# Performance work log

Measured on AMD Instinct MI355X. Metric: run time of the kernel, lower is better.

The kernel has to match this reference:

```python
import jax, jax.numpy as jnp
import numpy as np

ALPHA = 0.2  # tf.nn.leaky_relu default alpha
B, LATENT, T, N = 8, 256, 128, 768
F, L, E = 4, 3, 12288


def _causal_conv1d(x, w, b):
    # x: [B,T,Cin], w: [K,Cin,Cout] -> causal pad left by K-1
    k = w.shape[0]
    y = jax.lax.conv_general_dilated(x, w, (1,), ((k - 1, 0),),
                                     dimension_numbers=('NWC', 'WIO', 'NWC'))
    return y + b


def _same_conv1d(x, w, b):
    y = jax.lax.conv_general_dilated(x, w, (1,), 'SAME',
                                     dimension_numbers=('NWC', 'WIO', 'NWC'))
    return y + b


def _same_conv2d(x, w, b):
    y = jax.lax.conv_general_dilated(x, w, (1, 1), 'SAME',
                                     dimension_numbers=('NHWC', 'HWIO', 'NHWC'))
    return y + b


def _gat(nodes, row, col, qw, qb, kw, kb, vw, vb):
    # tf_geometric-style single-head GAT; row/col already contain self-loops.
    M = nodes.shape[0]
    Q = jax.nn.leaky_relu(nodes @ qw + qb, ALPHA)
    K = jax.nn.leaky_relu(nodes @ kw + kb, ALPHA)
    V = nodes @ vw
    scale = jnp.sqrt(jnp.asarray(Q.shape[-1], nodes.dtype))
    score = jnp.sum(Q[row] * K[col], axis=-1) / scale  # [E']
    smax = jax.ops.segment_max(score, row, num_segments=M)
    ex = jnp.exp(score - smax[row])
    den = jax.ops.segment_sum(ex, row, num_segments=M)
    att = ex / den[row]
    out = jax.ops.segment_sum(V[col] * att[:, None], row, num_segments=M)
    return out + vb


def _gw_layer(y, row, col, wa, ba, wb, bb, qw, qb, kw, kb, vw, vb, rw, rb):
    b_, t_, n_, f_ = y.shape
    x = jnp.moveaxis(y, -1, 0)  # [F,B,T,N]

    def branch(xf, wa_, ba_, wb_, bb_, qw_, qb_, kw_, kb_, vw_, vb_):
        a = jax.nn.sigmoid(_causal_conv1d(xf, wa_, ba_))
        g = a * jnp.tanh(_causal_conv1d(xf, wb_, bb_))   # gated TCN [B,T,N]
        nodes = g.transpose(0, 2, 1).reshape(b_ * n_, t_)  # node id = b*N + n
        h = _gat(nodes, row, col, qw_, qb_, kw_, kb_, vw_, vb_)
        return h.reshape(b_, n_, t_).transpose(0, 2, 1)  # [B,T,N]

    outs = jax.vmap(branch)(x, wa, ba, wb, bb, qw, qb, kw, kb, vw, vb)
    outs = jnp.moveaxis(outs, 0, -1)                      # [B,T,N,F]
    res = jnp.einsum('btnf,fg->btng', y, rw) + rb         # 1x1 res conv
    return outs + res


def _decoder(x, edges, shunt_dense_w, shunt_dense_b, shunt_c1_w, shunt_c1_b,
             shunt_c2_w, shunt_c2_b, tcn_a_w, tcn_a_b, tcn_b_w, tcn_b_b,
             gat_q_w, gat_q_b, gat_k_w, gat_k_b, gat_v_w, gat_v_b,
             res_w, res_b, skip_w, skip_b, out1_w, out1_b, out2_w, out2_b):
    # ConvShunt: [B,latent] -> [B,T] -> [B,T,N] -> [B,T,N,F]
    y = x @ shunt_dense_w + shunt_dense_b
    y = _same_conv1d(y[..., None], shunt_c1_w, shunt_c1_b)
    y = _same_conv2d(y[..., None], shunt_c2_w, shunt_c2_b)
    M = B * N
    self_idx = jnp.arange(M, dtype=edges.dtype)
    row = jnp.concatenate([edges[0], self_idx])
    col = jnp.concatenate([edges[1], self_idx])
    skips = []
    for i in range(L):
        y = _gw_layer(y, row, col, tcn_a_w[i], tcn_a_b[i], tcn_b_w[i], tcn_b_b[i],
                      gat_q_w[i], gat_q_b[i], gat_k_w[i], gat_k_b[i],
                      gat_v_w[i], gat_v_b[i], res_w[i], res_b[i])
        skips.append(jax.nn.leaky_relu(
            jnp.einsum('btnf,f->btn', y, skip_w[i]) + skip_b[i], ALPHA))
    s = jnp.stack(skips, axis=-1)                         # [B,T,N,L]
    g = jax.nn.leaky_relu(_same_conv2d(s, out1_w, out1_b), ALPHA)
    return _same_conv2d(g, out2_w, out2_b)                # [B,T,N,1]


def setup_inputs() -> dict:
    ks = iter(jax.random.split(jax.random.key(0), 32))

    def w(shape, fan_in):
        return jax.random.normal(next(ks), shape, jnp.float32) / np.sqrt(fan_in).astype(np.float32)

    return {
        'x': jax.random.normal(next(ks), (B, LATENT), jnp.float32),
        'edges': jax.random.randint(next(ks), (2, E), 0, N, jnp.int32),
        'shunt_dense_w': w((LATENT, T), LATENT),
        'shunt_dense_b': jnp.zeros((T,), jnp.float32),
        'shunt_c1_w': w((3, 1, N), 3),
        'shunt_c1_b': jnp.zeros((N,), jnp.float32),
        'shunt_c2_w': w((3, 3, 1, F), 9),
        'shunt_c2_b': jnp.zeros((F,), jnp.float32),
        'tcn_a_w': w((L, F, 5, N, N), 5 * N),
        'tcn_a_b': jnp.zeros((L, F, N), jnp.float32),
        'tcn_b_w': w((L, F, 5, N, N), 5 * N),
        'tcn_b_b': jnp.zeros((L, F, N), jnp.float32),
        'gat_q_w': w((L, F, T, T), T),
        'gat_q_b': jnp.zeros((L, F, T), jnp.float32),
        'gat_k_w': w((L, F, T, T), T),
        'gat_k_b': jnp.zeros((L, F, T), jnp.float32),
        'gat_v_w': w((L, F, T, T), T),
        'gat_v_b': jnp.zeros((L, F, T), jnp.float32),
        'res_w': w((L, F, F), F),
        'res_b': jnp.zeros((L, F), jnp.float32),
        'skip_w': w((L, F), F),
        'skip_b': jnp.zeros((L,), jnp.float32),
        'out1_w': w((3, 3, L, 1), 9 * L),
        'out1_b': jnp.zeros((1,), jnp.float32),
        'out2_w': w((1, 1, 1, 1), 1),
        'out2_b': jnp.zeros((1,), jnp.float32),
    }


def reference(x, edges, shunt_dense_w, shunt_dense_b, shunt_c1_w, shunt_c1_b,
              shunt_c2_w, shunt_c2_b, tcn_a_w, tcn_a_b, tcn_b_w, tcn_b_b,
              gat_q_w, gat_q_b, gat_k_w, gat_k_b, gat_v_w, gat_v_b,
              res_w, res_b, skip_w, skip_b, out1_w, out1_b, out2_w, out2_b):
    return _decoder(x, edges, shunt_dense_w, shunt_dense_b, shunt_c1_w, shunt_c1_b,
                    shunt_c2_w, shunt_c2_b, tcn_a_w, tcn_a_b, tcn_b_w, tcn_b_b,
                    gat_q_w, gat_q_b, gat_k_w, gat_k_b, gat_v_w, gat_v_b,
                    res_w, res_b, skip_w, skip_b, out1_w, out1_b, out2_w, out2_b)
```

## Files before the change

### kernel.cpp

```cpp
#include <hip/hip_runtime.h>
#include <math.h>

#define ALPHA_ 0.2f
#define AS1 __attribute__((address_space(1)))
#define AS3 __attribute__((address_space(3)))

constexpr int B_ = 8, LATENT_ = 256, T_ = 128, N_ = 768, F_ = 4, L_ = 3, E_ = 12288;
constexpr int M_ = B_ * N_;
constexpr int MT_ = B_ * T_;
constexpr int EP_ = E_ + M_;
constexpr int BTN_ = B_ * T_ * N_;
constexpr size_t SZ_ = (size_t)BTN_ * F_;
constexpr int KTCN_ = 5 * N_;
constexpr int KSPLIT_ = KTCN_ / 2;
constexpr int TP_ = T_ + 4;

typedef __bf16 bf16x8 __attribute__((ext_vector_type(8)));
typedef float f32x4 __attribute__((ext_vector_type(4)));

__device__ __forceinline__ float lrelu(float x) { return x > 0.0f ? x : ALPHA_ * x; }
__device__ __forceinline__ unsigned short f2bf(float x) {
    union { __bf16 h; unsigned short u; } c; c.h = (__bf16)x; return c.u;
}

__global__ void k_dense(const float* __restrict__ x, const float* __restrict__ w,
                        const float* __restrict__ b, float* __restrict__ y0) {
    int i = blockIdx.x * blockDim.x + threadIdx.x;
    if (i >= B_ * T_) return;
    int bb = i / T_, t = i % T_;
    float acc = b[t];
    for (int l = 0; l < LATENT_; ++l) acc += x[bb * LATENT_ + l] * w[l * T_ + t];
    y0[i] = acc;
}

__global__ void k_conv1(const float* __restrict__ y0, const float* __restrict__ w,
                        const float* __restrict__ b, float* __restrict__ y1) {
    int i = blockIdx.x * blockDim.x + threadIdx.x;
    if (i >= BTN_) return;
    int n = i % N_, t = (i / N_) % T_, bb = i / (N_ * T_);
    float acc = b[n];
    #pragma unroll
    for (int k = 0; k < 3; ++k) {
        int tt = t - 1 + k;
        if (tt >= 0 && tt < T_) acc += y0[bb * T_ + tt] * w[k * N_ + n];
    }
    y1[i] = acc;
}

__global__ void k_conv2w(const float* __restrict__ y1, const float* __restrict__ w,
                         const float* __restrict__ b, float* __restrict__ y,
                         unsigned short* __restrict__ xTpad) {
    int i = blockIdx.x * blockDim.x + threadIdx.x;
    if (i >= BTN_) return;
    int n = i % N_, t = (i / N_) % T_, bb = i / (N_ * T_);
    float acc[F_];
    #pragma unroll
    for (int f = 0; f < F_; ++f) acc[f] = b[f];
    #pragma unroll
    for (int dt = 0; dt < 3; ++dt) {
        int tt = t - 1 + dt;
        if (tt < 0 || tt >= T_) continue;
        #pragma unroll
        for (int dn = 0; dn < 3; ++dn) {
            int nn = n - 1 + dn;
            if (nn < 0 || nn >= N_) continue;
            float v = y1[(bb * T_ + tt) * N_ + nn];
            #pragma unroll
            for (int f = 0; f < F_; ++f) acc[f] += v * w[(dt * 3 + dn) * F_ + f];
        }
    }
    #pragma unroll
    for (int f = 0; f < F_; ++f) {
        y[(size_t)i * F_ + f] = acc[f];
        xTpad[((size_t)(f * B_ + bb) * TP_ + 4 + t) * N_ + n] = f2bf(acc[f]);
    }
}

__global__ __launch_bounds__(256) void k_convT(const float* __restrict__ in,
        unsigned short* __restrict__ outT, int Kd, int Nd) {
    __shared__ float tl[32][33];
    const int f = blockIdx.z;
    in += (size_t)f * Kd * Nd;
    outT += (size_t)f * Kd * Nd;
    const int x0 = blockIdx.x * 32;
    const int y0 = blockIdx.y * 32;
    const int tx = threadIdx.x & 31, ty = threadIdx.x >> 5;
    #pragma unroll
    for (int r = 0; r < 4; ++r)
        tl[ty + r * 8][tx] = in[(size_t)(y0 + ty + r * 8) * Nd + x0 + tx];
    __syncthreads();
    #pragma unroll
    for (int r = 0; r < 4; ++r)
        outT[(size_t)(x0 + ty + r * 8) * Kd + y0 + tx] = f2bf(tl[tx][ty + r * 8]);
}

__global__ __launch_bounds__(256) void k_tcn_mfma(
        const unsigned short* __restrict__ xTpad,
        const unsigned short* __restrict__ wat, const unsigned short* __restrict__ wbt,
        const float* __restrict__ ba, const float* __restrict__ bbias,
        float* __restrict__ oa0, float* __restrict__ oa1,
        float* __restrict__ ob0, float* __restrict__ ob1) {
    __shared__ unsigned short As[128 * 32];
    __shared__ unsigned short Bs[128 * 32];
    const int zz = blockIdx.z;
    const int f = zz & 3;
    const int wsel = (zz >> 2) & 1;
    const int s = zz >> 3;
    const int n0 = blockIdx.x * 128;
    const int bt = blockIdx.y;
    const unsigned short* xf = xTpad + (size_t)(f * B_ + bt) * TP_ * N_;
    const unsigned short* wf = (wsel ? wbt : wat) + (size_t)f * N_ * KTCN_ + (size_t)n0 * KTCN_;
    const float* bias = (wsel ? bbias : ba) + f * N_;
    float* out = (wsel ? (s ? ob1 : ob0) : (s ? oa1 : oa0));
    const int tid = threadIdx.x;
    const int lane = tid & 63;
    const int w = tid >> 6;
    const int wm = (w >> 1) * 64, wn = (w & 1) * 64;
    const int r16 = lane & 15, kb = lane >> 4;
    const int srow = lane >> 2;
    const int scol = (lane & 3) * 8;
    f32x4 acc[4][4] = {};
    const int k_lo = s * KSPLIT_, k_hi = k_lo + KSPLIT_;
    for (int kk0 = k_lo; kk0 < k_hi; kk0 += 32) {
        const int ks = kk0 / N_;
        const int nin0 = kk0 - ks * N_;
        #pragma unroll
        for (int h = 0; h < 2; ++h) {
            const int seg = w + 4 * h;
            const int row = seg * 16 + srow;
            const unsigned short* gA = xf + (size_t)(row + ks) * N_ + nin0 + scol;
            const unsigned short* gB = wf + (size_t)row * KTCN_ + kk0 + scol;
            __builtin_amdgcn_global_load_lds((const AS1 unsigned int*)(const void*)gA,
                    (AS3 unsigned int*)(void*)(As + seg * 512), 16, 0, 0);
            __builtin_amdgcn_global_load_lds((const AS1 unsigned int*)(const void*)gB,
                    (AS3 unsigned int*)(void*)(Bs + seg * 512), 16, 0, 0);
        }
        __syncthreads();
        bf16x8 av[4], bv[4];
        #pragma unroll
        for (int i = 0; i < 4; ++i) av[i] = *(const bf16x8*)(As + (wm + i * 16 + r16) * 32 + kb * 8);
        #pragma unroll
        for (int j = 0; j < 4; ++j) bv[j] = *(const bf16x8*)(Bs + (wn + j * 16 + r16) * 32 + kb * 8);
        #pragma unroll
        for (int i = 0; i < 4; ++i)
            #pragma unroll
            for (int j = 0; j < 4; ++j)
                acc[i][j] = __builtin_amdgcn_mfma_f32_16x16x32_bf16(av[i], bv[j], acc[i][j], 0, 0, 0);
        __syncthreads();
    }
    float* of = out + (size_t)(f * B_ + bt) * T_ * N_;
    #pragma unroll
    for (int i = 0; i < 4; ++i) {
        #pragma unroll
        for (int j = 0; j < 4; ++j) {
            const int n = n0 + wn + j * 16 + r16;
            const float bv2 = (s == 0) ? bias[n] : 0.0f;
            #pragma unroll
            for (int r = 0; r < 4; ++r) {
                const int m = wm + i * 16 + kb * 4 + r;
                of[(size_t)m * N_ + n] = acc[i][j][r] + bv2;
            }
        }
    }
}

__global__ __launch_bounds__(256) void k_gate_nodes(const float* __restrict__ a0,
        const float* __restrict__ a1, const float* __restrict__ b0,
        const float* __restrict__ b1, unsigned short* __restrict__ nodes) {
    __shared__ float tl[32][33];
    const int bz = blockIdx.z;
    const int t0 = blockIdx.x * 32, n0 = blockIdx.y * 32;
    const int tx = threadIdx.x & 31, ty = threadIdx.x >> 5;
    const size_t base = (size_t)bz * T_ * N_;
    #pragma unroll
    for (int r = 0; r < 4; ++r) {
        const size_t idx = base + (size_t)(t0 + ty + r * 8) * N_ + n0 + tx;
        const float av = a0[idx] + a1[idx], bvv = b0[idx] + b1[idx];
        tl[ty + r * 8][tx] = (1.0f / (1.0f + __expf(-av))) * tanhf(bvv);
    }
    __syncthreads();
    #pragma unroll
    for (int r = 0; r < 4; ++r)
        nodes[base + (size_t)(n0 + ty + r * 8) * T_ + t0 + tx] = f2bf(tl[tx][ty + r * 8]);
}

__global__ __launch_bounds__(256) void k_proj_mfma(
        const unsigned short* __restrict__ nodes, const unsigned short* __restrict__ pwt,
        const float* __restrict__ qb, const float* __restrict__ kbias,
        float* __restrict__ Q, float* __restrict__ K, float* __restrict__ V) {
    __shared__ unsigned short As[128 * 32];
    __shared__ unsigned short Bs[128 * 32];
    const int zz = blockIdx.z;
    const int f = zz & 3;
    const int sel = zz >> 2;
    const int m0 = blockIdx.y * 128;
    const unsigned short* af = nodes + (size_t)f * M_ * T_;
    const unsigned short* wfp = pwt + (size_t)sel * F_ * T_ * T_ + (size_t)f * T_ * T_;
    const float* bias = (sel == 0) ? qb : (sel == 1 ? kbias : nullptr);
    float* out = (sel == 0) ? Q : (sel == 1 ? K : V);
    const int tid = threadIdx.x;
    const int lane = tid & 63;
    const int w = tid >> 6;
    const int wm = (w >> 1) * 64, wn = (w & 1) * 64;
    const int r16 = lane & 15, kb = lane >> 4;
    const int srow = lane >> 2;
    const int scol = (lane & 3) * 8;
    f32x4 acc[4][4] = {};
    for (int kk0 = 0; kk0 < T_; kk0 += 32) {
        #pragma unroll
        for (int h = 0; h < 2; ++h) {
            const int seg = w + 4 * h;
            const int row = seg * 16 + srow;
            const unsigned short* gA = af + (size_t)(m0 + row) * T_ + kk0 + scol;
            const unsigned short* gB = wfp + (size_t)row * T_ + kk0 + scol;
            __builtin_amdgcn_global_load_lds((const AS1 unsigned int*)(const void*)gA,
                    (AS3 unsigned int*)(void*)(As + seg * 512), 16, 0, 0);
            __builtin_amdgcn_global_load_lds((const AS1 unsigned int*)(const void*)gB,
                    (AS3 unsigned int*)(void*)(Bs + seg * 512), 16, 0, 0);
        }
        __syncthreads();
        bf16x8 av[4], bv[4];
        #pragma unroll
        for (int i = 0; i < 4; ++i) av[i] = *(const bf16x8*)(As + (wm + i * 16 + r16) * 32 + kb * 8);
        #pragma unroll
        for (int j = 0; j < 4; ++j) bv[j] = *(const bf16x8*)(Bs + (wn + j * 16 + r16) * 32 + kb * 8);
        #pragma unroll
        for (int i = 0; i < 4; ++i)
            #pragma unroll
            for (int j = 0; j < 4; ++j)
                acc[i][j] = __builtin_amdgcn_mfma_f32_16x16x32_bf16(av[i], bv[j], acc[i][j], 0, 0, 0);
        __syncthreads();
    }
    const int do_l = (sel < 2);
    float* of = out + (size_t)f * M_ * T_;
    #pragma unroll
    for (int i = 0; i < 4; ++i) {
        #pragma unroll
        for (int j = 0; j < 4; ++j) {
            const int n = wn + j * 16 + r16;
            #pragma unroll
            for (int r = 0; r < 4; ++r) {
                const int m = m0 + wm + i * 16 + kb * 4 + r;
                float v = acc[i][j][r];
                if (bias) v += bias[f * T_ + n];
                if (do_l) v = lrelu(v);
                of[(size_t)m * T_ + n] = v;
            }
        }
    }
}

__device__ __forceinline__ int edge_row(const int* e, int i) { return i < E_ ? e[i] : i - E_; }
__device__ __forceinline__ int edge_col(const int* e, int i) { return i < E_ ? e[E_ + i] : i - E_; }

__global__ void k_hist(const int* __restrict__ edges, int* __restrict__ deg) {
    int i = blockIdx.x * blockDim.x + threadIdx.x;
    if (i >= EP_) return;
    atomicAdd(&deg[edge_row(edges, i)], 1);
}

__global__ __launch_bounds__(256) void k_scan(const int* __restrict__ deg,
        int* __restrict__ rowptr, int* __restrict__ cursor) {
    __shared__ int part[256];
    const int tid = threadIdx.x;
    constexpr int PER = M_ / 256;
    int loc[PER];
    int s = 0;
    #pragma unroll
    for (int j = 0; j < PER; ++j) { loc[j] = s; s += deg[tid * PER + j]; }
    part[tid] = s;
    __syncthreads();
    if (tid == 0) {
        int run = 0;
        for (int i2 = 0; i2 < 256; ++i2) { int v = part[i2]; part[i2] = run; run += v; }
        rowptr[M_] = run;
    }
    __syncthreads();
    const int off = part[tid];
    #pragma unroll
    for (int j = 0; j < PER; ++j) {
        rowptr[tid * PER + j] = off + loc[j];
        cursor[tid * PER + j] = off + loc[j];
    }
}

__global__ void k_scatter(const int* __restrict__ edges, int* __restrict__ cursor,
                          int* __restrict__ csr_col) {
    int i = blockIdx.x * blockDim.x + threadIdx.x;
    if (i >= EP_) return;
    int r = edge_row(edges, i), c = edge_col(edges, i);
    int pos = atomicAdd(&cursor[r], 1);
    csr_col[pos] = c;
}

__global__ __launch_bounds__(256) void k_gat(const float* __restrict__ Q,
        const float* __restrict__ Kb, const float* __restrict__ V,
        const int* __restrict__ rowptr, const int* __restrict__ csr_col,
        float* __restrict__ H) {
    constexpr int CAP = 128;
    __shared__ float sc[4][CAP];
    const int w = threadIdx.x >> 6, lane = threadIdx.x & 63;
    const int wv = blockIdx.x * 4 + w;
    const int f = wv / M_, r = wv - f * M_;
    const int p0 = rowptr[r], p1 = rowptr[r + 1];
    const float* Qr = Q + ((size_t)f * M_ + r) * T_;
    const float q0 = Qr[lane], q1 = Qr[lane + 64];
    float mx = -3.4e38f;
    for (int j = p0; j < p1; ++j) {
        const float* Kc = Kb + ((size_t)f * M_ + csr_col[j]) * T_;
        float s = q0 * Kc[lane] + q1 * Kc[lane + 64];
        #pragma unroll
        for (int mk = 32; mk >= 1; mk >>= 1) s += __shfl_xor(s, mk);
        s *= 0.0883883476483184f;
        if (lane == 0 && j - p0 < CAP) sc[w][j - p0] = s;
        mx = fmaxf(mx, s);
    }
    float den = 0.0f;
    for (int j = p0; j < p1; ++j) {
        float s;
        if (j - p0 < CAP) s = sc[w][j - p0];
        else {
            const float* Kc = Kb + ((size_t)f * M_ + csr_col[j]) * T_;
            s = q0 * Kc[lane] + q1 * Kc[lane + 64];
            #pragma unroll
            for (int mk = 32; mk >= 1; mk >>= 1) s += __shfl_xor(s, mk);
            s *= 0.0883883476483184f;
        }
        den += __expf(s - mx);
    }
    const float rden = 1.0f / den;
    float a0 = 0.0f, a1 = 0.0f;
    for (int j = p0; j < p1; ++j) {
        const int c = csr_col[j];
        float s;
        if (j - p0 < CAP) s = sc[w][j - p0];
        else {
            const float* Kc = Kb + ((size_t)f * M_ + c) * T_;
            s = q0 * Kc[lane] + q1 * Kc[lane + 64];
            #pragma unroll
            for (int mk = 32; mk >= 1; mk >>= 1) s += __shfl_xor(s, mk);
            s *= 0.0883883476483184f;
        }
        const float att = __expf(s - mx) * rden;
        const float* Vc = V + ((size_t)f * M_ + c) * T_;
        a0 += att * Vc[lane];
        a1 += att * Vc[lane + 64];
    }
    float* Hr = H + ((size_t)f * M_ + r) * T_;
    Hr[lane] = a0;
    Hr[lane + 64] = a1;
}

__global__ __launch_bounds__(256) void k_combine_t(const float* __restrict__ y,
        const float* __restrict__ H, const float* __restrict__ vb,
        const float* __restrict__ rw, const float* __restrict__ rb,
        const float* __restrict__ skw, const float* __restrict__ skb, int layer,
        float* __restrict__ ynext, unsigned short* __restrict__ xTpad,
        float* __restrict__ sbufp) {
    __shared__ float hl[F_][32][33];
    const int b = blockIdx.z;
    const int t0 = blockIdx.x * 32, n0 = blockIdx.y * 32;
    const int tx = threadIdx.x & 31, ty = threadIdx.x >> 5;
    #pragma unroll
    for (int g = 0; g < F_; ++g)
        #pragma unroll
        for (int r = 0; r < 4; ++r) {
            const int nn = ty + r * 8;
            hl[g][nn][tx] = H[((size_t)g * M_ + b * N_ + n0 + nn) * T_ + t0 + tx];
        }
    __syncthreads();
    #pragma unroll
    for (int r = 0; r < 4; ++r) {
        const int tt = ty + r * 8;
        const int t = t0 + tt;
        const size_t i = ((size_t)b * T_ + t) * N_ + n0 + tx;
        const float4 y4 = *(const float4*)(y + i * 4);
        float o[F_];
        #pragma unroll
        for (int g = 0; g < F_; ++g) {
            float acc = hl[g][tx][tt] + vb[g * T_ + t] + rb[g];
            acc += y4.x * rw[0 * F_ + g] + y4.y * rw[1 * F_ + g]
                 + y4.z * rw[2 * F_ + g] + y4.w * rw[3 * F_ + g];
            o[g] = acc;
        }
        float4 o4 = {o[0], o[1], o[2], o[3]};
        *(float4*)(ynext + i * 4) = o4;
        #pragma unroll
        for (int g = 0; g < F_; ++g)
            xTpad[((size_t)(g * B_ + b) * TP_ + 4 + t) * N_ + n0 + tx] = f2bf(o[g]);
        float sk = skb[layer];
        #pragma unroll
        for (int g = 0; g < F_; ++g) sk += o[g] * skw[layer * F_ + g];
        sbufp[(size_t)layer * BTN_ + i] = lrelu(sk);
    }
}

__global__ void k_final(const float* __restrict__ sbufp, const float* __restrict__ o1w,
        const float* __restrict__ o1b, const float* __restrict__ o2w,
        const float* __restrict__ o2b, float* __restrict__ out) {
    int i = blockIdx.x * blockDim.x + threadIdx.x;
    if (i >= BTN_) return;
    int n = i % N_, t = (i / N_) % T_, bb = i / (N_ * T_);
    float acc = o1b[0];
    #pragma unroll
    for (int dt = 0; dt < 3; ++dt) {
        int tt = t - 1 + dt;
        if (tt < 0 || tt >= T_) continue;
        #pragma unroll
        for (int dn = 0; dn < 3; ++dn) {
            int nn = n - 1 + dn;
            if (nn < 0 || nn >= N_) continue;
            const size_t base = (size_t)(bb * T_ + tt) * N_ + nn;
            #pragma unroll
            for (int l = 0; l < L_; ++l)
                acc += sbufp[(size_t)l * BTN_ + base] * o1w[(dt * 3 + dn) * L_ + l];
        }
    }
    float g = lrelu(acc);
    out[i] = g * o2w[0] + o2b[0];
}

extern "C" void kernel_launch(void* const* d_in, const int* in_sizes, int n_in,
                              void* d_out, int out_size, void* d_ws, size_t ws_size,
                              hipStream_t stream) {
    const float* x       = (const float*)d_in[0];
    const int*   edges   = (const int*)d_in[1];
    const float* sd_w    = (const float*)d_in[2];
    const float* sd_b    = (const float*)d_in[3];
    const float* c1w     = (const float*)d_in[4];
    const float* c1b     = (const float*)d_in[5];
    const float* c2w     = (const float*)d_in[6];
    const float* c2b     = (const float*)d_in[7];
    const float* tcn_a_w = (const float*)d_in[8];
    const float* tcn_a_b = (const float*)d_in[9];
    const float* tcn_b_w = (const float*)d_in[10];
    const float* tcn_b_b = (const float*)d_in[11];
    const float* gat_q_w = (const float*)d_in[12];
    const float* gat_q_b = (const float*)d_in[13];
    const float* gat_k_w = (const float*)d_in[14];
    const float* gat_k_b = (const float*)d_in[15];
    const float* gat_v_w = (const float*)d_in[16];
    const float* gat_v_b = (const float*)d_in[17];
    const float* res_w   = (const float*)d_in[18];
    const float* res_b   = (const float*)d_in[19];
    const float* skip_w  = (const float*)d_in[20];
    const float* skip_b  = (const float*)d_in[21];
    const float* out1_w  = (const float*)d_in[22];
    const float* out1_b  = (const float*)d_in[23];
    const float* out2_w  = (const float*)d_in[24];
    const float* out2_b  = (const float*)d_in[25];
    float* out = (float*)d_out;

    float* ws = (float*)d_ws;
    size_t off = 0;
    auto alloc = [&](size_t nf) { float* p = ws + off; off += nf; return p; };
    float* ybuf  = alloc(SZ_);
    float* y2buf = alloc(SZ_);
    float* H     = alloc(SZ_);
    float* apre  = alloc(SZ_);
    float* bpre  = alloc(SZ_);
    float* V     = alloc(SZ_);
    float* sbufp = alloc((size_t)BTN_ * L_);
    float* y0    = alloc(MT_);
    float* y1    = alloc(BTN_);
    unsigned short* xTpad  = (unsigned short*)alloc((size_t)F_ * B_ * TP_ * N_ / 2 + 16);
    unsigned short* nodesb = (unsigned short*)alloc(SZ_ / 2);
    unsigned short* wat = (unsigned short*)alloc((size_t)F_ * KTCN_ * N_ / 2);
    unsigned short* wbt = (unsigned short*)alloc((size_t)F_ * KTCN_ * N_ / 2);
    unsigned short* pwt = (unsigned short*)alloc((size_t)3 * F_ * T_ * T_ / 2);
    int* rowptr  = (int*)alloc(M_ + 1);
    int* cursor  = (int*)alloc(M_);
    int* deg     = (int*)alloc(M_);
    int* csr_col = (int*)alloc(EP_);
    (void)ws_size; (void)in_sizes; (void)n_in; (void)out_size;

    hipMemsetAsync(xTpad, 0, (size_t)F_ * B_ * TP_ * N_ * 2, stream);
    hipMemsetAsync(deg, 0, M_ * 4, stream);
    k_hist<<<(EP_ + 255) / 256, 256, 0, stream>>>(edges, deg);
    k_scan<<<1, 256, 0, stream>>>(deg, rowptr, cursor);
    k_scatter<<<(EP_ + 255) / 256, 256, 0, stream>>>(edges, cursor, csr_col);

    k_dense<<<(B_ * T_ + 255) / 256, 256, 0, stream>>>(x, sd_w, sd_b, y0);
    k_conv1<<<(BTN_ + 255) / 256, 256, 0, stream>>>(y0, c1w, c1b, y1);
    k_conv2w<<<(BTN_ + 255) / 256, 256, 0, stream>>>(y1, c2w, c2b, ybuf, xTpad);

    float* cur = ybuf;
    float* nxt = y2buf;
    for (int layer = 0; layer < L_; ++layer) {
        const float* wa = tcn_a_w + (size_t)layer * F_ * KTCN_ * N_;
        const float* ba = tcn_a_b + (size_t)layer * F_ * N_;
        const float* wb = tcn_b_w + (size_t)layer * F_ * KTCN_ * N_;
        const float* bb = tcn_b_b + (size_t)layer * F_ * N_;
        const float* qw = gat_q_w + (size_t)layer * F_ * T_ * T_;
        const float* qb = gat_q_b + (size_t)layer * F_ * T_;
        const float* kw = gat_k_w + (size_t)layer * F_ * T_ * T_;
        const float* kbias = gat_k_b + (size_t)layer * F_ * T_;
        const float* vw = gat_v_w + (size_t)layer * F_ * T_ * T_;
        const float* vb = gat_v_b + (size_t)layer * F_ * T_;
        const float* rw = res_w + (size_t)layer * F_ * F_;
        const float* rb = res_b + (size_t)layer * F_;

        dim3 gw(N_ / 32, KTCN_ / 32, F_);
        k_convT<<<gw, 256, 0, stream>>>(wa, wat, KTCN_, N_);
        k_convT<<<gw, 256, 0, stream>>>(wb, wbt, KTCN_, N_);
        dim3 gt(N_ / 128, B_, 16);
        k_tcn_mfma<<<gt, 256, 0, stream>>>(xTpad, wat, wbt, ba, bb, apre, V, bpre, H);
        dim3 gg(T_ / 32, N_ / 32, F_ * B_);
        k_gate_nodes<<<gg, 256, 0, stream>>>(apre, V, bpre, H, nodesb);
        dim3 gpw(T_ / 32, T_ / 32, F_);
        const int PWOFF = F_ * T_ * T_;
        k_convT<<<gpw, 256, 0, stream>>>(qw, pwt, T_, T_);
        k_convT<<<gpw, 256, 0, stream>>>(kw, pwt + PWOFF, T_, T_);
        k_convT<<<gpw, 256, 0, stream>>>(vw, pwt + 2 * PWOFF, T_, T_);
        dim3 gp(1, M_ / 128, 12);
        k_proj_mfma<<<gp, 256, 0, stream>>>(nodesb, pwt, qb, kbias, apre, bpre, V);
        k_gat<<<(F_ * M_) / 4, 256, 0, stream>>>(apre, bpre, V, rowptr, csr_col, H);
        dim3 gc(T_ / 32, N_ / 32, B_);
        k_combine_t<<<gc, 256, 0, stream>>>(cur, H, vb, rw, rb, skip_w, skip_b,
                layer, nxt, xTpad, sbufp);
        float* tmp = cur; cur = nxt; nxt = tmp;
    }
    k_final<<<(BTN_ + 255) / 256, 256, 0, stream>>>(sbufp, out1_w, out1_b, out2_w, out2_b, out);
}
```

Before: 607.6 us.

## Store GAT Q/K/V in bf16, swizzle LDS, shrink TCN N-tile, fuse weight transposes

The Q/K/V projections are now written as bf16 and converted back in the GAT kernel, which halves the gather traffic per edge. The LDS tiles in the TCN and projection GEMMs use an XOR swizzle to cut bank conflicts. The TCN GEMM tile drops from 128 to 64 along N, doubling the number of blocks. The two TCN weight transposes are merged into one launch with 64-row tiles. In exchange, attention inputs carry lower precision, and the narrower tile reuses the A operand less.

```diff
diff --git a/kernel.cpp b/kernel.cpp
--- a/kernel.cpp
+++ b/kernel.cpp
@@ -22,6 +22,9 @@
 __device__ __forceinline__ unsigned short f2bf(float x) {
     union { __bf16 h; unsigned short u; } c; c.h = (__bf16)x; return c.u;
 }
+__device__ __forceinline__ float bf2f(unsigned short u) {
+    return __uint_as_float(((unsigned)u) << 16);
+}
 
 __global__ void k_dense(const float* __restrict__ x, const float* __restrict__ w,
                         const float* __restrict__ b, float* __restrict__ y0) {
@@ -94,6 +97,26 @@
         outT[(size_t)(x0 + ty + r * 8) * Kd + y0 + tx] = f2bf(tl[tx][ty + r * 8]);
 }
 
+__global__ __launch_bounds__(256) void k_convT2(const float* __restrict__ in0,
+        const float* __restrict__ in1, unsigned short* __restrict__ out0,
+        unsigned short* __restrict__ out1) {
+    __shared__ float tl[64][33];
+    const int z = blockIdx.z;
+    const int f = z & 3, wsel = z >> 2;
+    const float* in = (wsel ? in1 : in0) + (size_t)f * KTCN_ * N_;
+    unsigned short* outT = (wsel ? out1 : out0) + (size_t)f * KTCN_ * N_;
+    const int n0 = blockIdx.x * 32, k0 = blockIdx.y * 64;
+    const int tx = threadIdx.x & 31, ty = threadIdx.x >> 5;
+    #pragma unroll
+    for (int r = 0; r < 8; ++r)
+        tl[ty + r * 8][tx] = in[(size_t)(k0 + ty + r * 8) * N_ + n0 + tx];
+    __syncthreads();
+    const int kx2 = threadIdx.x & 63, ny = threadIdx.x >> 6;
+    #pragma unroll
+    for (int r = 0; r < 8; ++r)
+        outT[(size_t)(n0 + ny + r * 4) * KTCN_ + k0 + kx2] = f2bf(tl[kx2][ny + r * 4]);
+}
+
 __global__ __launch_bounds__(256) void k_tcn_mfma(
         const unsigned short* __restrict__ xTpad,
         const unsigned short* __restrict__ wat, const unsigned short* __restrict__ wbt,
@@ -101,12 +124,12 @@
         float* __restrict__ oa0, float* __restrict__ oa1,
         float* __restrict__ ob0, float* __restrict__ ob1) {
     __shared__ unsigned short As[128 * 32];
-    __shared__ unsigned short Bs[128 * 32];
+    __shared__ unsigned short Bs[64 * 32];
     const int zz = blockIdx.z;
     const int f = zz & 3;
     const int wsel = (zz >> 2) & 1;
     const int s = zz >> 3;
-    const int n0 = blockIdx.x * 128;
+    const int n0 = blockIdx.x * 64;
     const int bt = blockIdx.y;
     const unsigned short* xf = xTpad + (size_t)(f * B_ + bt) * TP_ * N_;
     const unsigned short* wf = (wsel ? wbt : wat) + (size_t)f * N_ * KTCN_ + (size_t)n0 * KTCN_;
@@ -115,11 +138,12 @@
     const int tid = threadIdx.x;
     const int lane = tid & 63;
     const int w = tid >> 6;
-    const int wm = (w >> 1) * 64, wn = (w & 1) * 64;
+    const int wm = (w >> 1) * 64, wn = (w & 1) * 32;
     const int r16 = lane & 15, kb = lane >> 4;
     const int srow = lane >> 2;
-    const int scol = (lane & 3) * 8;
-    f32x4 acc[4][4] = {};
+    const int scol = (((lane & 3) ^ ((lane >> 3) & 3)) * 8);
+    const int kx = (kb ^ ((r16 >> 1) & 3)) * 8;
+    f32x4 acc[4][2] = {};
     const int k_lo = s * KSPLIT_, k_hi = k_lo + KSPLIT_;
     for (int kk0 = k_lo; kk0 < k_hi; kk0 += 32) {
         const int ks = kk0 / N_;
@@ -129,22 +153,24 @@
             const int seg = w + 4 * h;
             const int row = seg * 16 + srow;
             const unsigned short* gA = xf + (size_t)(row + ks) * N_ + nin0 + scol;
-            const unsigned short* gB = wf + (size_t)row * KTCN_ + kk0 + scol;
             __builtin_amdgcn_global_load_lds((const AS1 unsigned int*)(const void*)gA,
                     (AS3 unsigned int*)(void*)(As + seg * 512), 16, 0, 0);
-            __builtin_amdgcn_global_load_lds((const AS1 unsigned int*)(const void*)gB,
-                    (AS3 unsigned int*)(void*)(Bs + seg * 512), 16, 0, 0);
+            if (h == 0) {
+                const unsigned short* gB = wf + (size_t)row * KTCN_ + kk0 + scol;
+                __builtin_amdgcn_global_load_lds((const AS1 unsigned int*)(const void*)gB,
+                        (AS3 unsigned int*)(void*)(Bs + seg * 512), 16, 0, 0);
+            }
         }
         __syncthreads();
-        bf16x8 av[4], bv[4];
-        #pragma unroll
-        for (int i = 0; i < 4; ++i) av[i] = *(const bf16x8*)(As + (wm + i * 16 + r16) * 32 + kb * 8);
-        #pragma unroll
-        for (int j = 0; j < 4; ++j) bv[j] = *(const bf16x8*)(Bs + (wn + j * 16 + r16) * 32 + kb * 8);
+        bf16x8 av[4], bv[2];
+        #pragma unroll
+        for (int i = 0; i < 4; ++i) av[i] = *(const bf16x8*)(As + (wm + i * 16 + r16) * 32 + kx);
+        #pragma unroll
+        for (int j = 0; j < 2; ++j) bv[j] = *(const bf16x8*)(Bs + (wn + j * 16 + r16) * 32 + kx);
         #pragma unroll
         for (int i = 0; i < 4; ++i)
             #pragma unroll
-            for (int j = 0; j < 4; ++j)
+            for (int j = 0; j < 2; ++j)
                 acc[i][j] = __builtin_amdgcn_mfma_f32_16x16x32_bf16(av[i], bv[j], acc[i][j], 0, 0, 0);
         __syncthreads();
     }
@@ -152,7 +178,7 @@
     #pragma unroll
     for (int i = 0; i < 4; ++i) {
         #pragma unroll
-        for (int j = 0; j < 4; ++j) {
+        for (int j = 0; j < 2; ++j) {
             const int n = n0 + wn + j * 16 + r16;
             const float bv2 = (s == 0) ? bias[n] : 0.0f;
             #pragma unroll
@@ -187,7 +213,8 @@
 __global__ __launch_bounds__(256) void k_proj_mfma(
         const unsigned short* __restrict__ nodes, const unsigned short* __restrict__ pwt,
         const float* __restrict__ qb, const float* __restrict__ kbias,
-        float* __restrict__ Q, float* __restrict__ K, float* __restrict__ V) {
+        unsigned short* __restrict__ Q, unsigned short* __restrict__ K,
+        unsigned short* __restrict__ V) {
     __shared__ unsigned short As[128 * 32];
     __shared__ unsigned short Bs[128 * 32];
     const int zz = blockIdx.z;
@@ -197,14 +224,15 @@
     const unsigned short* af = nodes + (size_t)f * M_ * T_;
     const unsigned short* wfp = pwt + (size_t)sel * F_ * T_ * T_ + (size_t)f * T_ * T_;
     const float* bias = (sel == 0) ? qb : (sel == 1 ? kbias : nullptr);
-    float* out = (sel == 0) ? Q : (sel == 1 ? K : V);
+    unsigned short* out = (sel == 0) ? Q : (sel == 1 ? K : V);
     const int tid = threadIdx.x;
     const int lane = tid & 63;
     const int w = tid >> 6;
     const int wm = (w >> 1) * 64, wn = (w & 1) * 64;
     const int r16 = lane & 15, kb = lane >> 4;
     const int srow = lane >> 2;
-    const int scol = (lane & 3) * 8;
+    const int scol = (((lane & 3) ^ ((lane >> 3) & 3)) * 8);
+    const int kx = (kb ^ ((r16 >> 1) & 3)) * 8;
     f32x4 acc[4][4] = {};
     for (int kk0 = 0; kk0 < T_; kk0 += 32) {
         #pragma unroll
@@ -221,9 +249,9 @@
         __syncthreads();
         bf16x8 av[4], bv[4];
         #pragma unroll
-        for (int i = 0; i < 4; ++i) av[i] = *(const bf16x8*)(As + (wm + i * 16 + r16) * 32 + kb * 8);
-        #pragma unroll
-        for (int j = 0; j < 4; ++j) bv[j] = *(const bf16x8*)(Bs + (wn + j * 16 + r16) * 32 + kb * 8);
+        for (int i = 0; i < 4; ++i) av[i] = *(const bf16x8*)(As + (wm + i * 16 + r16) * 32 + kx);
+        #pragma unroll
+        for (int j = 0; j < 4; ++j) bv[j] = *(const bf16x8*)(Bs + (wn + j * 16 + r16) * 32 + kx);
         #pragma unroll
         for (int i = 0; i < 4; ++i)
             #pragma unroll
@@ -232,7 +260,7 @@
         __syncthreads();
     }
     const int do_l = (sel < 2);
-    float* of = out + (size_t)f * M_ * T_;
+    unsigned short* of = out + (size_t)f * M_ * T_;
     #pragma unroll
     for (int i = 0; i < 4; ++i) {
         #pragma unroll
@@ -244,7 +272,7 @@
                 float v = acc[i][j][r];
                 if (bias) v += bias[f * T_ + n];
                 if (do_l) v = lrelu(v);
-                of[(size_t)m * T_ + n] = v;
+                of[(size_t)m * T_ + n] = f2bf(v);
             }
         }
     }
@@ -293,8 +321,8 @@
     csr_col[pos] = c;
 }
 
-__global__ __launch_bounds__(256) void k_gat(const float* __restrict__ Q,
-        const float* __restrict__ Kb, const float* __restrict__ V,
+__global__ __launch_bounds__(256) void k_gat(const unsigned short* __restrict__ Q,
+        const unsigned short* __restrict__ Kb, const unsigned short* __restrict__ V,
         const int* __restrict__ rowptr, const int* __restrict__ csr_col,
         float* __restrict__ H) {
     constexpr int CAP = 128;
@@ -303,12 +331,12 @@
     const int wv = blockIdx.x * 4 + w;
     const int f = wv / M_, r = wv - f * M_;
     const int p0 = rowptr[r], p1 = rowptr[r + 1];
-    const float* Qr = Q + ((size_t)f * M_ + r) * T_;
-    const float q0 = Qr[lane], q1 = Qr[lane + 64];
+    const unsigned short* Qr = Q + ((size_t)f * M_ + r) * T_;
+    const float q0 = bf2f(Qr[lane]), q1 = bf2f(Qr[lane + 64]);
     float mx = -3.4e38f;
     for (int j = p0; j < p1; ++j) {
-        const float* Kc = Kb + ((size_t)f * M_ + csr_col[j]) * T_;
-        float s = q0 * Kc[lane] + q1 * Kc[lane + 64];
+        const unsigned short* Kc = Kb + ((size_t)f * M_ + csr_col[j]) * T_;
+        float s = q0 * bf2f(Kc[lane]) + q1 * bf2f(Kc[lane + 64]);
         #pragma unroll
         for (int mk = 32; mk >= 1; mk >>= 1) s += __shfl_xor(s, mk);
         s *= 0.0883883476483184f;
@@ -320,8 +348,8 @@
         float s;
         if (j - p0 < CAP) s = sc[w][j - p0];
         else {
-            const float* Kc = Kb + ((size_t)f * M_ + csr_col[j]) * T_;
-            s = q0 * Kc[lane] + q1 * Kc[lane + 64];
+            const unsigned short* Kc = Kb + ((size_t)f * M_ + csr_col[j]) * T_;
+            s = q0 * bf2f(Kc[lane]) + q1 * bf2f(Kc[lane + 64]);
             #pragma unroll
             for (int mk = 32; mk >= 1; mk >>= 1) s += __shfl_xor(s, mk);
             s *= 0.0883883476483184f;
@@ -335,16 +363,16 @@
         float s;
         if (j - p0 < CAP) s = sc[w][j - p0];
         else {
-            const float* Kc = Kb + ((size_t)f * M_ + c) * T_;
-            s = q0 * Kc[lane] + q1 * Kc[lane + 64];
+            const unsigned short* Kc = Kb + ((size_t)f * M_ + c) * T_;
+            s = q0 * bf2f(Kc[lane]) + q1 * bf2f(Kc[lane + 64]);
             #pragma unroll
             for (int mk = 32; mk >= 1; mk >>= 1) s += __shfl_xor(s, mk);
             s *= 0.0883883476483184f;
         }
         const float att = __expf(s - mx) * rden;
-        const float* Vc = V + ((size_t)f * M_ + c) * T_;
-        a0 += att * Vc[lane];
-        a1 += att * Vc[lane + 64];
+        const unsigned short* Vc = V + ((size_t)f * M_ + c) * T_;
+        a0 += att * bf2f(Vc[lane]);
+        a1 += att * bf2f(Vc[lane + 64]);
     }
     float* Hr = H + ((size_t)f * M_ + r) * T_;
     Hr[lane] = a0;
@@ -465,6 +493,9 @@
     float* y1    = alloc(BTN_);
     unsigned short* xTpad  = (unsigned short*)alloc((size_t)F_ * B_ * TP_ * N_ / 2 + 16);
     unsigned short* nodesb = (unsigned short*)alloc(SZ_ / 2);
+    unsigned short* qb16   = (unsigned short*)alloc(SZ_ / 2);
+    unsigned short* kb16   = (unsigned short*)alloc(SZ_ / 2);
+    unsigned short* vb16   = (unsigned short*)alloc(SZ_ / 2);
     unsigned short* wat = (unsigned short*)alloc((size_t)F_ * KTCN_ * N_ / 2);
     unsigned short* wbt = (unsigned short*)alloc((size_t)F_ * KTCN_ * N_ / 2);
     unsigned short* pwt = (unsigned short*)alloc((size_t)3 * F_ * T_ * T_ / 2);
@@ -500,10 +531,9 @@
         const float* rw = res_w + (size_t)layer * F_ * F_;
         const float* rb = res_b + (size_t)layer * F_;
 
-        dim3 gw(N_ / 32, KTCN_ / 32, F_);
-        k_convT<<<gw, 256, 0, stream>>>(wa, wat, KTCN_, N_);
-        k_convT<<<gw, 256, 0, stream>>>(wb, wbt, KTCN_, N_);
-        dim3 gt(N_ / 128, B_, 16);
+        dim3 gw2(N_ / 32, KTCN_ / 64, 2 * F_);
+        k_convT2<<<gw2, 256, 0, stream>>>(wa, wb, wat, wbt);
+        dim3 gt(N_ / 64, B_, 16);
         k_tcn_mfma<<<gt, 256, 0, stream>>>(xTpad, wat, wbt, ba, bb, apre, V, bpre, H);
         dim3 gg(T_ / 32, N_ / 32, F_ * B_);
         k_gate_nodes<<<gg, 256, 0, stream>>>(apre, V, bpre, H, nodesb);
@@ -513,8 +543,8 @@
         k_convT<<<gpw, 256, 0, stream>>>(kw, pwt + PWOFF, T_, T_);
         k_convT<<<gpw, 256, 0, stream>>>(vw, pwt + 2 * PWOFF, T_, T_);
         dim3 gp(1, M_ / 128, 12);
-        k_proj_mfma<<<gp, 256, 0, stream>>>(nodesb, pwt, qb, kbias, apre, bpre, V);
-        k_gat<<<(F_ * M_) / 4, 256, 0, stream>>>(apre, bpre, V, rowptr, csr_col, H);
+        k_proj_mfma<<<gp, 256, 0, stream>>>(nodesb, pwt, qb, kbias, qb16, kb16, vb16);
+        k_gat<<<(F_ * M_) / 4, 256, 0, stream>>>(qb16, kb16, vb16, rowptr, csr_col, H);
         dim3 gc(T_ / 32, N_ / 32, B_);
         k_combine_t<<<gc, 256, 0, stream>>>(cur, H, vb, rw, rb, skip_w, skip_b,
                 layer, nxt, xTpad, sbufp);
```

Measured after the change: 716.1 us. +17.8%, slower.
